# Optimization experiments

Hardware: AMD Instinct MI355X
Metric: run time of the kernel (lower is better)

## Reference

```python
import jax, jax.numpy as jnp
import numpy as np

N = 50000
E = 800000
IN_C, HID, OUT_C, HEADS = 128, 32, 64, 4
NEG_SLOPE = 0.2


def setup_inputs() -> dict:
    key = jax.random.key(0)
    ks = jax.random.split(key, 10)
    x = jax.random.normal(ks[0], (N, IN_C), dtype=jnp.float32)
    edge_index = jax.random.randint(ks[1], (2, E), 0, N, dtype=jnp.int64)
    s = 0.05
    W1 = jax.random.normal(ks[2], (IN_C, HID), dtype=jnp.float32) * s
    b1 = jnp.zeros((HID,), dtype=jnp.float32)
    Wg = jax.random.normal(ks[3], (HID, HEADS * HID), dtype=jnp.float32) * s
    ag_src = jax.random.normal(ks[4], (HEADS, HID), dtype=jnp.float32) * s
    ag_dst = jax.random.normal(ks[5], (HEADS, HID), dtype=jnp.float32) * s
    bg = jnp.zeros((HID,), dtype=jnp.float32)
    W2 = jax.random.normal(ks[6], (HID, OUT_C), dtype=jnp.float32) * s
    b2 = jnp.zeros((OUT_C,), dtype=jnp.float32)
    return {"x": x, "edge_index": edge_index, "W1": W1, "b1": b1,
            "Wg": Wg, "ag_src": ag_src, "ag_dst": ag_dst, "bg": bg,
            "W2": W2, "b2": b2}


def _add_self_loops(edge_index, n):
    loop = jnp.arange(n, dtype=edge_index.dtype)
    return jnp.concatenate([edge_index, jnp.stack([loop, loop])], axis=1)


def _gcn(x, src, dst, W, b, n):
    # PyG GCNConv: symmetric normalization with self-loops, scatter-add
    xw = x @ W  # [N, F]
    deg = jnp.zeros((n,), xw.dtype).at[dst].add(1.0)  # in-degree incl self-loops
    dinv = jax.lax.rsqrt(deg)
    norm = dinv[src] * dinv[dst]  # [E']
    msg = xw[src] * norm[:, None]  # [E', F]
    out = jax.ops.segment_sum(msg, dst, num_segments=n)
    return out + b


def _gat(x, src, dst, Wg, a_src, a_dst, b, n):
    # PyG GATConv, concat=False (mean over heads), leaky_relu slope 0.2
    h = (x @ Wg).reshape(n, HEADS, HID)  # [N, H, D]
    al_s = jnp.einsum('nhd,hd->nh', h, a_src)  # [N, H]
    al_d = jnp.einsum('nhd,hd->nh', h, a_dst)
    logits = jax.nn.leaky_relu(al_s[src] + al_d[dst], NEG_SLOPE)  # [E', H]
    # segment softmax over incoming edges of each dst node
    m = jax.ops.segment_max(logits, dst, num_segments=n)
    e = jnp.exp(logits - m[dst])
    denom = jax.ops.segment_sum(e, dst, num_segments=n)
    alpha = e / denom[dst]  # [E', H]
    msg = h[src] * alpha[:, :, None]  # [E', H, D]
    out = jax.ops.segment_sum(msg, dst, num_segments=n)  # [N, H, D]
    return out.mean(axis=1) + b


def reference(x, edge_index, W1, b1, Wg, ag_src, ag_dst, bg, W2, b2):
    ei = _add_self_loops(edge_index, N)
    src, dst = ei[0], ei[1]
    h = jax.nn.relu(_gcn(x, src, dst, W1, b1, N))
    h = jax.nn.relu(_gat(h, src, dst, Wg, ag_src, ag_dst, bg, N))
    return _gcn(h, src, dst, W2, b2, N)
```

## Files before the change

### kernel.cpp

```cpp
#include <hip/hip_runtime.h>
#include <hip/hip_bf16.h>

#define N_NODES 50000
#define N_EDGES 800000
#define EP (N_EDGES + N_NODES)
#define IN_C 128
#define HID 32
#define OUT_C 64
#define HEADS 4
#define NEG_SLOPE 0.2f

#define NPB 128
#define K_BUCKETS ((N_NODES + NPB - 1) / NPB)

typedef unsigned int uint32;
typedef __attribute__((ext_vector_type(8))) short bf16x8;
typedef __attribute__((ext_vector_type(4))) float f32x4;

__device__ __forceinline__ float bf_lo(uint32 u) { return __uint_as_float(u << 16); }
__device__ __forceinline__ float bf_hi(uint32 u) { return __uint_as_float(u & 0xffff0000u); }
__device__ __forceinline__ uint32 f2bf(float f) {
    uint32 u = __float_as_uint(f);
    return (u + 0x7fffu + ((u >> 16) & 1u)) >> 16;
}
__device__ __forceinline__ uint32 pack_bf2(float a, float b) {
    return f2bf(a) | (f2bf(b) << 16);
}

__global__ __launch_bounds__(512) void k_init2(int* __restrict__ gcnt,
                                               const float* __restrict__ Wg,
                                               const float* __restrict__ ags,
                                               const float* __restrict__ agd,
                                               float* __restrict__ wals,
                                               float* __restrict__ wald,
                                               const float* __restrict__ W2,
                                               uint32* __restrict__ wgB,
                                               uint32* __restrict__ w2B) {
    int t = threadIdx.x;
    if (t < K_BUCKETS + 1) gcnt[t] = 0;
    if (t < 256) {
        int c = t & 127;
        int h = c >> 5, k = c & 31;
        const float* a = (t < 128) ? ags : agd;
        float acc = 0.f;
#pragma unroll
        for (int d = 0; d < 32; d++) acc += Wg[k * 128 + h * 32 + d] * a[h * 32 + d];
        if (t < 128) wals[c] = acc; else wald[c] = acc;
    }
    for (int i = t; i < 2048; i += 512) {
        int tile = i >> 8;
        int T = tile >> 2, kt = tile & 3;
        int r = i & 255;
        int L = r >> 2, di = r & 3;
        int k0 = kt * 32 + (L >> 4) * 8 + 2 * di;
        int k1 = k0 + 1;
        int n = T * 16 + (L & 15);
        float a = Wg[(k0 & 31) * 128 + (k0 >> 5) * 32 + n];
        float b = Wg[(k1 & 31) * 128 + (k1 >> 5) * 32 + n];
        wgB[i] = pack_bf2(a, b);
    }
    for (int i = t; i < 1024; i += 512) {
        int T = i >> 8;
        int r = i & 255;
        int L = r >> 2, di = r & 3;
        int k0 = (L >> 4) * 8 + 2 * di;
        int n = T * 16 + (L & 15);
        w2B[i] = pack_bf2(W2[k0 * 64 + n], W2[(k0 + 1) * 64 + n]);
    }
}


__global__ __launch_bounds__(256) void k_bcount(const int* __restrict__ ei,
                                                int* __restrict__ gcnt) {
    __shared__ int h[K_BUCKETS];
    int t = threadIdx.x;
    for (int i = t; i < K_BUCKETS; i += 256) h[i] = 0;
    __syncthreads();
    int base = blockIdx.x * 4096;
    int dd[16];
#pragma unroll
    for (int k = 0; k < 16; k++) {
        int e = base + k * 256 + t;
        dd[k] = (e < N_EDGES) ? ei[N_EDGES + e] : -1;
    }
#pragma unroll
    for (int k = 0; k < 16; k++)
        if (dd[k] >= 0) atomicAdd(&h[dd[k] >> 7], 1);
    __syncthreads();
    for (int i = t; i < K_BUCKETS; i += 256)
        if (h[i]) atomicAdd(&gcnt[i], h[i]);
}

__global__ __launch_bounds__(512) void k_bscan(const int* __restrict__ gcnt,
                                               int* __restrict__ gbase,
                                               int* __restrict__ gcursor) {
    __shared__ int sd[512];
    int t = threadIdx.x;
    int v = (t < K_BUCKETS) ? gcnt[t] : 0;
    sd[t] = v;
    __syncthreads();
    for (int off = 1; off < 512; off <<= 1) {
        int x = (t >= off) ? sd[t - off] : 0;
        __syncthreads();
        sd[t] += x;
        __syncthreads();
    }
    if (t < K_BUCKETS) {
        int excl = sd[t] - v;
        gbase[t] = excl;
        gcursor[t] = excl;
    }
    if (t == 0) gbase[K_BUCKETS] = sd[K_BUCKETS - 1];
}

__global__ __launch_bounds__(256) void k_bucket(const int* __restrict__ ei,
                                                int* __restrict__ gcursor,
                                                uint32* __restrict__ gpairs) {
    __shared__ int cnt[K_BUCKETS];
    __shared__ int bas[K_BUCKETS];
    int t = threadIdx.x;
    for (int i = t; i < K_BUCKETS; i += 256) cnt[i] = 0;
    __syncthreads();
    int base = blockIdx.x * 2048;
    int ss[8], dd[8], ml[8];
#pragma unroll
    for (int k = 0; k < 8; k++) {
        int e = base + k * 256 + t;
        ss[k] = (e < N_EDGES) ? ei[e] : -1;
        dd[k] = (e < N_EDGES) ? ei[N_EDGES + e] : 0;
    }
#pragma unroll
    for (int k = 0; k < 8; k++)
        if (ss[k] >= 0) ml[k] = atomicAdd(&cnt[dd[k] >> 7], 1);
    __syncthreads();
    for (int i = t; i < K_BUCKETS; i += 256)
        bas[i] = cnt[i] ? atomicAdd(&gcursor[i], cnt[i]) : 0;
    __syncthreads();
#pragma unroll
    for (int k = 0; k < 8; k++)
        if (ss[k] >= 0)
            gpairs[bas[dd[k] >> 7] + ml[k]] = ((uint32)ss[k] << 7) | (uint32)(dd[k] & 127);
}

__global__ __launch_bounds__(256) void k_node(const uint32* __restrict__ gpairs,
                                              const int* __restrict__ gbase,
                                              int* __restrict__ offs,
                                              float* __restrict__ dinv,
                                              int* __restrict__ srcs,
                                              int* __restrict__ perm) {
    __shared__ int cnt[NPB];
    __shared__ int scn[NPB];
    __shared__ int cur[NPB];
    __shared__ unsigned skey[NPB];
    int t = threadIdx.x;
    int b = blockIdx.x;
    int lo = b << 7;
    int nn = N_NODES - lo; if (nn > NPB) nn = NPB;
    int pb = gbase[b], pe = gbase[b + 1];
    if (t < NPB) cnt[t] = 0;
    __syncthreads();
    for (int i = pb + t; i < pe; i += 256)
        atomicAdd(&cnt[gpairs[i] & 127], 1);
    __syncthreads();
    if (t < NPB) scn[t] = cnt[t];
    __syncthreads();
    for (int off = 1; off < NPB; off <<= 1) {
        int x = 0;
        if (t >= off && t < NPB) x = scn[t - off];
        __syncthreads();
        if (t < NPB) scn[t] += x;
        __syncthreads();
    }
    if (t < nn) {
        int excl = scn[t] - cnt[t];
        int o = pb + excl + lo + t;
        offs[lo + t] = o;
        cur[t] = o;
        dinv[lo + t] = rsqrtf((float)(cnt[t] + 1));
        srcs[pb + scn[t] + lo + t] = lo + t;
    }
    if (b == K_BUCKETS - 1 && t == 0) offs[N_NODES] = pe + N_NODES;
    __syncthreads();
    for (int i = pb + t; i < pe; i += 256) {
        uint32 u = gpairs[i];
        int pos = atomicAdd(&cur[u & 127], 1);
        srcs[pos] = (int)(u >> 7);
    }
    if (t < NPB)
        skey[t] = (t < nn) ? (((unsigned)cnt[t] << 7) | (unsigned)t)
                           : (0x7fffff80u | (unsigned)t);
    __syncthreads();
    for (int k = 2; k <= NPB; k <<= 1) {
        for (int jj = k >> 1; jj > 0; jj >>= 1) {
            if (t < NPB) {
                int ixj = t ^ jj;
                if (ixj > t) {
                    unsigned a = skey[t], bb = skey[ixj];
                    if (((t & k) == 0) ? (a > bb) : (a < bb)) {
                        skey[t] = bb; skey[ixj] = a;
                    }
                }
            }
            __syncthreads();
        }
    }
    if (t < nn) perm[lo + t] = lo + (int)(skey[t] & 127u);
}

__global__ __launch_bounds__(256) void k_gemm1(const float* __restrict__ x,
                                               const float* __restrict__ W1,
                                               const float* __restrict__ dinv,
                                               uint32* __restrict__ xw1) {
    __shared__ float wl[IN_C * HID];
    __shared__ float xl[8 * IN_C];
    int t = threadIdx.x;
    for (int i = t; i < IN_C * HID; i += 256) {
        int k = i >> 5, f = i & 31;
        wl[(k >> 1) * 64 + f * 2 + (k & 1)] = W1[i];
    }
    int nb = blockIdx.x * 8;
    const float4* x4 = (const float4*)(x + (size_t)nb * IN_C);
    ((float4*)xl)[t] = x4[t];
    __syncthreads();
    int g = t >> 5, f = t & 31;
    const float2* xr = (const float2*)(xl + g * IN_C);
    const float2* wp = (const float2*)wl;
    float acc = 0.f;
#pragma unroll 16
    for (int k2 = 0; k2 < 64; k2++) {
        float2 xv = xr[k2];
        float2 wv = wp[k2 * 32 + f];
        acc += xv.x * wv.x + xv.y * wv.y;
    }
    float v = acc * dinv[nb + g];
    float vn = __shfl_xor(v, 1, 64);
    if ((f & 1) == 0) xw1[(size_t)(nb + g) * 16 + (f >> 1)] = pack_bf2(v, vn);
}

__global__ __launch_bounds__(256) void k_gather1(const uint32* __restrict__ xw1,
                                                 const int* __restrict__ offs,
                                                 const int* __restrict__ srcs,
                                                 const int* __restrict__ perm,
                                                 const float* __restrict__ dinv,
                                                 const float* __restrict__ b1,
                                                 const float* __restrict__ wals,
                                                 const float* __restrict__ wald,
                                                 char* __restrict__ rec) {
    int t = threadIdx.x;
    int l16 = t & 15;
    int n = perm[blockIdx.x * 16 + (t >> 4)];
    int s0 = offs[n], s1 = offs[n + 1];
    const char* xb = (const char*)xw1 + l16 * 4;
    float a0 = 0.f, a1 = 0.f, a2 = 0.f, a3 = 0.f;
    float a4 = 0.f, a5 = 0.f, a6 = 0.f, a7 = 0.f;
    int j = s0;
    for (; j + 3 < s1; j += 4) {
        uint32 uA = *(const uint32*)(xb + ((uint32)srcs[j] << 6));
        uint32 uB = *(const uint32*)(xb + ((uint32)srcs[j + 1] << 6));
        uint32 uC = *(const uint32*)(xb + ((uint32)srcs[j + 2] << 6));
        uint32 uD = *(const uint32*)(xb + ((uint32)srcs[j + 3] << 6));
        a0 += bf_lo(uA); a1 += bf_hi(uA);
        a2 += bf_lo(uB); a3 += bf_hi(uB);
        a4 += bf_lo(uC); a5 += bf_hi(uC);
        a6 += bf_lo(uD); a7 += bf_hi(uD);
    }
    for (; j < s1; ++j) {
        uint32 uA = *(const uint32*)(xb + ((uint32)srcs[j] << 6));
        a0 += bf_lo(uA); a1 += bf_hi(uA);
    }
    float dn = dinv[n];
    float2 b = ((const float2*)b1)[l16];
    float vx = ((a0 + a2) + (a4 + a6)) * dn + b.x;
    float vy = ((a1 + a3) + (a5 + a7)) * dn + b.y;
    vx = vx > 0.f ? vx : 0.f;
    vy = vy > 0.f ? vy : 0.f;
    char* rn = rec + (size_t)n * 128;
    *(uint32*)(rn + l16 * 4) = pack_bf2(vx, vy);

    float ps0, ps1, ps2, ps3, pd0, pd1, pd2, pd3;
    {
        float2 w0 = ((const float2*)wals)[0 * 16 + l16];
        float2 w1 = ((const float2*)wals)[1 * 16 + l16];
        float2 w2 = ((const float2*)wals)[2 * 16 + l16];
        float2 w3 = ((const float2*)wals)[3 * 16 + l16];
        ps0 = vx * w0.x + vy * w0.y;
        ps1 = vx * w1.x + vy * w1.y;
        ps2 = vx * w2.x + vy * w2.y;
        ps3 = vx * w3.x + vy * w3.y;
        float2 u0 = ((const float2*)wald)[0 * 16 + l16];
        float2 u1 = ((const float2*)wald)[1 * 16 + l16];
        float2 u2 = ((const float2*)wald)[2 * 16 + l16];
        float2 u3 = ((const float2*)wald)[3 * 16 + l16];
        pd0 = vx * u0.x + vy * u0.y;
        pd1 = vx * u1.x + vy * u1.y;
        pd2 = vx * u2.x + vy * u2.y;
        pd3 = vx * u3.x + vy * u3.y;
    }
#pragma unroll
    for (int m = 1; m < 16; m <<= 1) {
        ps0 += __shfl_xor(ps0, m, 16); ps1 += __shfl_xor(ps1, m, 16);
        ps2 += __shfl_xor(ps2, m, 16); ps3 += __shfl_xor(ps3, m, 16);
        pd0 += __shfl_xor(pd0, m, 16); pd1 += __shfl_xor(pd1, m, 16);
        pd2 += __shfl_xor(pd2, m, 16); pd3 += __shfl_xor(pd3, m, 16);
    }
    if (l16 == 0) {
        float4* r4 = (float4*)rn;
        r4[4] = make_float4(ps0, ps1, ps2, ps3);
        r4[5] = make_float4(pd0, pd1, pd2, pd3);
    }
}

__global__ __launch_bounds__(512) void k_gat_agg(const char* __restrict__ rec,
                                                 const int* __restrict__ offs,
                                                 const int* __restrict__ srcs,
                                                 const int* __restrict__ perm,
                                                 const uint32* __restrict__ wgB,
                                                 const float* __restrict__ bg,
                                                 const float* __restrict__ dinv,
                                                 uint32* __restrict__ h2s) {
    __shared__ __align__(16) uint32 gl[16][64];
    int t = threadIdx.x;
    int l32 = t & 31;
    int g8 = t >> 5;
    int n = perm[blockIdx.x * 16 + g8];
    int l16 = l32 & 15;
    int par = l32 >> 4;
    int s0 = offs[n], s1 = offs[n + 1];
    float4 dv = ((const float4*)(rec + (size_t)n * 128))[5];
    uint32 hoff = l16 * 4;

    float g00 = 0.f, g01 = 0.f, g10 = 0.f, g11 = 0.f;
    float g20 = 0.f, g21 = 0.f, g30 = 0.f, g31 = 0.f;
    float ss0 = 0.f, ss1 = 0.f, ss2 = 0.f, ss3 = 0.f;

#define GAT_EDGE(J)                                                            \
    {                                                                          \
        uint32 off = (uint32)srcs[J] << 7;                                     \
        float4 ev = *(const float4*)(rec + off + 64);                          \
        uint32 u = *(const uint32*)(rec + off + hoff);                         \
        float flo = bf_lo(u), fhi = bf_hi(u);                                  \
        float tt, w;                                                           \
        tt = ev.x + dv.x; w = __expf(fmaxf(tt, NEG_SLOPE * tt));               \
        ss0 += w; g00 += w * flo; g01 += w * fhi;                              \
        tt = ev.y + dv.y; w = __expf(fmaxf(tt, NEG_SLOPE * tt));               \
        ss1 += w; g10 += w * flo; g11 += w * fhi;                              \
        tt = ev.z + dv.z; w = __expf(fmaxf(tt, NEG_SLOPE * tt));               \
        ss2 += w; g20 += w * flo; g21 += w * fhi;                              \
        tt = ev.w + dv.w; w = __expf(fmaxf(tt, NEG_SLOPE * tt));               \
        ss3 += w; g30 += w * flo; g31 += w * fhi;                              \
    }

    int j = s0 + par;
    for (; j + 2 < s1; j += 4) {
        GAT_EDGE(j);
        GAT_EDGE(j + 2);
    }
    if (j < s1) GAT_EDGE(j);
#undef GAT_EDGE

    ss0 += __shfl_xor(ss0, 16, 64); ss1 += __shfl_xor(ss1, 16, 64);
    ss2 += __shfl_xor(ss2, 16, 64); ss3 += __shfl_xor(ss3, 16, 64);
    g00 += __shfl_xor(g00, 16, 64); g01 += __shfl_xor(g01, 16, 64);
    g10 += __shfl_xor(g10, 16, 64); g11 += __shfl_xor(g11, 16, 64);
    g20 += __shfl_xor(g20, 16, 64); g21 += __shfl_xor(g21, 16, 64);
    g30 += __shfl_xor(g30, 16, 64); g31 += __shfl_xor(g31, 16, 64);
    float i0 = 0.25f / ss0, i1 = 0.25f / ss1, i2 = 0.25f / ss2, i3 = 0.25f / ss3;
    if (l32 < 16) {
        gl[g8][0 * 16 + l16] = pack_bf2(g00 * i0, g01 * i0);
        gl[g8][1 * 16 + l16] = pack_bf2(g10 * i1, g11 * i1);
        gl[g8][2 * 16 + l16] = pack_bf2(g20 * i2, g21 * i2);
        gl[g8][3 * 16 + l16] = pack_bf2(g30 * i3, g31 * i3);
    }
    __syncthreads();
    if (t < 64) {
        int L = t;
        int mA = L & 15;
        int quad = L >> 4;
        int nbase = blockIdx.x * 16;
        int pn[4];
        float dns[4];
#pragma unroll
        for (int r = 0; r < 4; r++) {
            pn[r] = perm[nbase + quad * 4 + r];
            dns[r] = dinv[pn[r]];
        }
#pragma unroll
        for (int T = 0; T < 2; T++) {
            f32x4 acc = {0.f, 0.f, 0.f, 0.f};
#pragma unroll
            for (int kt = 0; kt < 4; kt++) {
                bf16x8 af = *(const bf16x8*)&gl[mA][kt * 16 + quad * 4];
                bf16x8 bf = *(const bf16x8*)(wgB + (size_t)((T * 4 + kt) * 64 + L) * 4);
                acc = __builtin_amdgcn_mfma_f32_16x16x32_bf16(af, bf, acc, 0, 0, 0);
            }
            int d = T * 16 + (L & 15);
            float bgd = bg[d];
#pragma unroll
            for (int r = 0; r < 4; r++) {
                float v = acc[r] + bgd;
                v = v > 0.f ? v : 0.f;
                v *= dns[r];
                float vn = __shfl_xor(v, 1, 64);
                if ((d & 1) == 0)
                    h2s[(size_t)pn[r] * 16 + (d >> 1)] = pack_bf2(v, vn);
            }
        }
    }
}

__global__ __launch_bounds__(256) void k_gather2(const uint32* __restrict__ h2s,
                                                 const int* __restrict__ offs,
                                                 const int* __restrict__ srcs,
                                                 const int* __restrict__ perm,
                                                 const uint32* __restrict__ w2B,
                                                 const float* __restrict__ dinv,
                                                 const float* __restrict__ b2,
                                                 float* __restrict__ out) {
    __shared__ __align__(16) uint32 gbf[16][16];
    int t = threadIdx.x;
    int l16 = t & 15;
    int g16 = t >> 4;
    int n = perm[blockIdx.x * 16 + g16];
    int s0 = offs[n], s1 = offs[n + 1];
    const char* xb = (const char*)h2s + l16 * 4;
    float a0 = 0.f, a1 = 0.f, a2 = 0.f, a3 = 0.f;
    float a4 = 0.f, a5 = 0.f, a6 = 0.f, a7 = 0.f;
    int j = s0;
    for (; j + 3 < s1; j += 4) {
        uint32 uA = *(const uint32*)(xb + ((uint32)srcs[j] << 6));
        uint32 uB = *(const uint32*)(xb + ((uint32)srcs[j + 1] << 6));
        uint32 uC = *(const uint32*)(xb + ((uint32)srcs[j + 2] << 6));
        uint32 uD = *(const uint32*)(xb + ((uint32)srcs[j + 3] << 6));
        a0 += bf_lo(uA); a1 += bf_hi(uA);
        a2 += bf_lo(uB); a3 += bf_hi(uB);
        a4 += bf_lo(uC); a5 += bf_hi(uC);
        a6 += bf_lo(uD); a7 += bf_hi(uD);
    }
    for (; j < s1; ++j) {
        uint32 uA = *(const uint32*)(xb + ((uint32)srcs[j] << 6));
        a0 += bf_lo(uA); a1 += bf_hi(uA);
    }
    gbf[g16][l16] = pack_bf2((a0 + a2) + (a4 + a6), (a1 + a3) + (a5 + a7));
    __syncthreads();
    if (t < 64) {
        int L = t;
        int quad = L >> 4;
        int nbase = blockIdx.x * 16;
        int pn[4];
        float dns[4];
#pragma unroll
        for (int r = 0; r < 4; r++) {
            pn[r] = perm[nbase + quad * 4 + r];
            dns[r] = dinv[pn[r]];
        }
        bf16x8 af = *(const bf16x8*)&gbf[L & 15][quad * 4];
#pragma unroll
        for (int T = 0; T < 4; T++) {
            bf16x8 bf = *(const bf16x8*)(w2B + (size_t)(T * 64 + L) * 4);
            f32x4 acc = {0.f, 0.f, 0.f, 0.f};
            acc = __builtin_amdgcn_mfma_f32_16x16x32_bf16(af, bf, acc, 0, 0, 0);
            int d = T * 16 + (L & 15);
            float b2d = b2[d];
#pragma unroll
            for (int r = 0; r < 4; r++) {
                out[(size_t)pn[r] * OUT_C + d] = acc[r] * dns[r] + b2d;
            }
        }
    }
}

extern "C" void kernel_launch(void* const* d_in, const int* in_sizes, int n_in,
                              void* d_out, int out_size, void* d_ws, size_t ws_size,
                              hipStream_t stream) {
    const float* x   = (const float*)d_in[0];
    const int*   ei  = (const int*)d_in[1];
    const float* W1  = (const float*)d_in[2];
    const float* b1  = (const float*)d_in[3];
    const float* Wg  = (const float*)d_in[4];
    const float* ags = (const float*)d_in[5];
    const float* agd = (const float*)d_in[6];
    const float* bg  = (const float*)d_in[7];
    const float* W2  = (const float*)d_in[8];
    const float* b2  = (const float*)d_in[9];
    float* out = (float*)d_out;

    char* p = (char*)d_ws;
    auto alloc = [&](size_t bytes) -> void* {
        void* r = (void*)p;
        p += (bytes + 255) & ~(size_t)255;
        return r;
    };
    float*  dinv    = (float*)alloc((size_t)N_NODES * 4);
    int*    offs    = (int*)  alloc((size_t)(N_NODES + 1) * 4);
    int*    gcnt    = (int*)  alloc((size_t)(K_BUCKETS + 1) * 4);
    int*    gbase   = (int*)  alloc((size_t)(K_BUCKETS + 1) * 4);
    int*    gcursor = (int*)  alloc((size_t)(K_BUCKETS + 1) * 4);
    int*    srcs    = (int*)  alloc((size_t)EP * 4);
    uint32* gpairs  = (uint32*)alloc((size_t)N_EDGES * 4);
    uint32* xw1     = (uint32*)alloc((size_t)N_NODES * 16 * 4);
    char*   rec     = (char*) alloc((size_t)N_NODES * 128);
    float*  wals    = (float*)alloc(128 * 4);
    float*  wald    = (float*)alloc(128 * 4);
    uint32* wgB     = (uint32*)alloc(2048 * 4);
    uint32* w2B     = (uint32*)alloc(1024 * 4);
    uint32* h2s     = (uint32*)alloc((size_t)N_NODES * 16 * 4);
    int*    perm    = (int*)  alloc((size_t)N_NODES * 4);

    k_init2<<<1, 512, 0, stream>>>(gcnt, Wg, ags, agd, wals, wald, W2, wgB, w2B);
    k_bcount<<<(N_EDGES + 4095) / 4096, 256, 0, stream>>>(ei, gcnt);
    k_bscan<<<1, 512, 0, stream>>>(gcnt, gbase, gcursor);
    k_bucket<<<(N_EDGES + 2047) / 2048, 256, 0, stream>>>(ei, gcursor, gpairs);
    k_node<<<K_BUCKETS, 256, 0, stream>>>(gpairs, gbase, offs, dinv, srcs, perm);

    k_gemm1<<<N_NODES / 8, 256, 0, stream>>>(x, W1, dinv, xw1);
    k_gather1<<<N_NODES / 16, 256, 0, stream>>>(xw1, offs, srcs, perm, dinv, b1,
                                                wals, wald, rec);

    k_gat_agg<<<N_NODES / 16, 512, 0, stream>>>(rec, offs, srcs, perm, wgB, bg,
                                                dinv, h2s);

    k_gather2<<<N_NODES / 16, 256, 0, stream>>>(h2s, offs, srcs, perm, w2B,
                                                dinv, b2, out);
}
```

Baseline: 219.8 us.

## Vectorize neighbor gathers by splitting lanes across edges and feature chunks

The three gather kernels (GCN layer 1, GAT aggregation, GCN layer 2) now split each node's lane group between several edges in parallel and a feature slice per lane. Each lane issues 16-byte (GCN) or 8-byte (GAT) loads instead of 4-byte loads, and cross-edge partial sums are combined with shuffles. The aim is fewer, wider memory transactions per gathered row and more edges in flight at once, which matters for these latency-bound random gathers. In exchange it adds shuffle reductions, a predicated tail that reads srcs past the edge range (the buffer is padded to allow this), and more accumulator registers in the GAT kernel.

```diff
diff --git a/kernel.cpp b/kernel.cpp
--- a/kernel.cpp
+++ b/kernel.cpp
@@ -248,65 +248,67 @@
                                                  char* __restrict__ rec) {
     int t = threadIdx.x;
     int l16 = t & 15;
+    int es = l16 >> 2;
+    int q  = l16 & 3;
     int n = perm[blockIdx.x * 16 + (t >> 4)];
     int s0 = offs[n], s1 = offs[n + 1];
-    const char* xb = (const char*)xw1 + l16 * 4;
     float a0 = 0.f, a1 = 0.f, a2 = 0.f, a3 = 0.f;
     float a4 = 0.f, a5 = 0.f, a6 = 0.f, a7 = 0.f;
-    int j = s0;
-    for (; j + 3 < s1; j += 4) {
-        uint32 uA = *(const uint32*)(xb + ((uint32)srcs[j] << 6));
-        uint32 uB = *(const uint32*)(xb + ((uint32)srcs[j + 1] << 6));
-        uint32 uC = *(const uint32*)(xb + ((uint32)srcs[j + 2] << 6));
-        uint32 uD = *(const uint32*)(xb + ((uint32)srcs[j + 3] << 6));
-        a0 += bf_lo(uA); a1 += bf_hi(uA);
-        a2 += bf_lo(uB); a3 += bf_hi(uB);
-        a4 += bf_lo(uC); a5 += bf_hi(uC);
-        a6 += bf_lo(uD); a7 += bf_hi(uD);
-    }
-    for (; j < s1; ++j) {
-        uint32 uA = *(const uint32*)(xb + ((uint32)srcs[j] << 6));
-        a0 += bf_lo(uA); a1 += bf_hi(uA);
-    }
+#pragma unroll 2
+    for (int j = s0; j < s1; j += 4) {
+        int je = j + es;
+        int sidx = srcs[je];
+        if (je < s1) {
+            uint4 u = *(const uint4*)((const char*)xw1 + ((uint32)sidx << 6) + q * 16);
+            a0 += bf_lo(u.x); a1 += bf_hi(u.x);
+            a2 += bf_lo(u.y); a3 += bf_hi(u.y);
+            a4 += bf_lo(u.z); a5 += bf_hi(u.z);
+            a6 += bf_lo(u.w); a7 += bf_hi(u.w);
+        }
+    }
+#define RED_ES(v) v += __shfl_xor(v, 4, 64); v += __shfl_xor(v, 8, 64);
+    RED_ES(a0) RED_ES(a1) RED_ES(a2) RED_ES(a3)
+    RED_ES(a4) RED_ES(a5) RED_ES(a6) RED_ES(a7)
+#undef RED_ES
     float dn = dinv[n];
-    float2 b = ((const float2*)b1)[l16];
-    float vx = ((a0 + a2) + (a4 + a6)) * dn + b.x;
-    float vy = ((a1 + a3) + (a5 + a7)) * dn + b.y;
-    vx = vx > 0.f ? vx : 0.f;
-    vy = vy > 0.f ? vy : 0.f;
+    float4 bA = ((const float4*)b1)[2 * q];
+    float4 bB = ((const float4*)b1)[2 * q + 1];
+    float v0 = a0 * dn + bA.x, v1 = a1 * dn + bA.y;
+    float v2 = a2 * dn + bA.z, v3 = a3 * dn + bA.w;
+    float v4 = a4 * dn + bB.x, v5 = a5 * dn + bB.y;
+    float v6 = a6 * dn + bB.z, v7 = a7 * dn + bB.w;
+    v0 = v0 > 0.f ? v0 : 0.f; v1 = v1 > 0.f ? v1 : 0.f;
+    v2 = v2 > 0.f ? v2 : 0.f; v3 = v3 > 0.f ? v3 : 0.f;
+    v4 = v4 > 0.f ? v4 : 0.f; v5 = v5 > 0.f ? v5 : 0.f;
+    v6 = v6 > 0.f ? v6 : 0.f; v7 = v7 > 0.f ? v7 : 0.f;
     char* rn = rec + (size_t)n * 128;
-    *(uint32*)(rn + l16 * 4) = pack_bf2(vx, vy);
-
-    float ps0, ps1, ps2, ps3, pd0, pd1, pd2, pd3;
-    {
-        float2 w0 = ((const float2*)wals)[0 * 16 + l16];
-        float2 w1 = ((const float2*)wals)[1 * 16 + l16];
-        float2 w2 = ((const float2*)wals)[2 * 16 + l16];
-        float2 w3 = ((const float2*)wals)[3 * 16 + l16];
-        ps0 = vx * w0.x + vy * w0.y;
-        ps1 = vx * w1.x + vy * w1.y;
-        ps2 = vx * w2.x + vy * w2.y;
-        ps3 = vx * w3.x + vy * w3.y;
-        float2 u0 = ((const float2*)wald)[0 * 16 + l16];
-        float2 u1 = ((const float2*)wald)[1 * 16 + l16];
-        float2 u2 = ((const float2*)wald)[2 * 16 + l16];
-        float2 u3 = ((const float2*)wald)[3 * 16 + l16];
-        pd0 = vx * u0.x + vy * u0.y;
-        pd1 = vx * u1.x + vy * u1.y;
-        pd2 = vx * u2.x + vy * u2.y;
-        pd3 = vx * u3.x + vy * u3.y;
-    }
-#pragma unroll
-    for (int m = 1; m < 16; m <<= 1) {
-        ps0 += __shfl_xor(ps0, m, 16); ps1 += __shfl_xor(ps1, m, 16);
-        ps2 += __shfl_xor(ps2, m, 16); ps3 += __shfl_xor(ps3, m, 16);
-        pd0 += __shfl_xor(pd0, m, 16); pd1 += __shfl_xor(pd1, m, 16);
-        pd2 += __shfl_xor(pd2, m, 16); pd3 += __shfl_xor(pd3, m, 16);
+    if (es == 0) {
+        uint4 w;
+        w.x = pack_bf2(v0, v1); w.y = pack_bf2(v2, v3);
+        w.z = pack_bf2(v4, v5); w.w = pack_bf2(v6, v7);
+        *(uint4*)(rn + q * 16) = w;
+    }
+    float ps[4], pd[4];
+#pragma unroll
+    for (int h = 0; h < 4; h++) {
+        const float4* wa = (const float4*)(wals + h * 32 + 8 * q);
+        float4 wv0 = wa[0], wv1 = wa[1];
+        ps[h] = v0 * wv0.x + v1 * wv0.y + v2 * wv0.z + v3 * wv0.w
+              + v4 * wv1.x + v5 * wv1.y + v6 * wv1.z + v7 * wv1.w;
+        const float4* wb = (const float4*)(wald + h * 32 + 8 * q);
+        float4 uv0 = wb[0], uv1 = wb[1];
+        pd[h] = v0 * uv0.x + v1 * uv0.y + v2 * uv0.z + v3 * uv0.w
+              + v4 * uv1.x + v5 * uv1.y + v6 * uv1.z + v7 * uv1.w;
+    }
+#pragma unroll
+    for (int h = 0; h < 4; h++) {
+        ps[h] += __shfl_xor(ps[h], 1, 64); ps[h] += __shfl_xor(ps[h], 2, 64);
+        pd[h] += __shfl_xor(pd[h], 1, 64); pd[h] += __shfl_xor(pd[h], 2, 64);
     }
     if (l16 == 0) {
         float4* r4 = (float4*)rn;
-        r4[4] = make_float4(ps0, ps1, ps2, ps3);
-        r4[5] = make_float4(pd0, pd1, pd2, pd3);
+        r4[4] = make_float4(ps[0], ps[1], ps[2], ps[3]);
+        r4[5] = make_float4(pd[0], pd[1], pd[2], pd[3]);
     }
 }
 
@@ -323,53 +325,56 @@
     int l32 = t & 31;
     int g8 = t >> 5;
     int n = perm[blockIdx.x * 16 + g8];
-    int l16 = l32 & 15;
-    int par = l32 >> 4;
+    int es = l32 >> 3;
+    int q  = l32 & 7;
     int s0 = offs[n], s1 = offs[n + 1];
     float4 dv = ((const float4*)(rec + (size_t)n * 128))[5];
-    uint32 hoff = l16 * 4;
-
-    float g00 = 0.f, g01 = 0.f, g10 = 0.f, g11 = 0.f;
-    float g20 = 0.f, g21 = 0.f, g30 = 0.f, g31 = 0.f;
+
+    float g00 = 0.f, g01 = 0.f, g02 = 0.f, g03 = 0.f;
+    float g10 = 0.f, g11 = 0.f, g12 = 0.f, g13 = 0.f;
+    float g20 = 0.f, g21 = 0.f, g22 = 0.f, g23 = 0.f;
+    float g30 = 0.f, g31 = 0.f, g32 = 0.f, g33 = 0.f;
     float ss0 = 0.f, ss1 = 0.f, ss2 = 0.f, ss3 = 0.f;
 
-#define GAT_EDGE(J)                                                            \
-    {                                                                          \
-        uint32 off = (uint32)srcs[J] << 7;                                     \
-        float4 ev = *(const float4*)(rec + off + 64);                          \
-        uint32 u = *(const uint32*)(rec + off + hoff);                         \
-        float flo = bf_lo(u), fhi = bf_hi(u);                                  \
-        float tt, w;                                                           \
-        tt = ev.x + dv.x; w = __expf(fmaxf(tt, NEG_SLOPE * tt));               \
-        ss0 += w; g00 += w * flo; g01 += w * fhi;                              \
-        tt = ev.y + dv.y; w = __expf(fmaxf(tt, NEG_SLOPE * tt));               \
-        ss1 += w; g10 += w * flo; g11 += w * fhi;                              \
-        tt = ev.z + dv.z; w = __expf(fmaxf(tt, NEG_SLOPE * tt));               \
-        ss2 += w; g20 += w * flo; g21 += w * fhi;                              \
-        tt = ev.w + dv.w; w = __expf(fmaxf(tt, NEG_SLOPE * tt));               \
-        ss3 += w; g30 += w * flo; g31 += w * fhi;                              \
-    }
-
-    int j = s0 + par;
-    for (; j + 2 < s1; j += 4) {
-        GAT_EDGE(j);
-        GAT_EDGE(j + 2);
-    }
-    if (j < s1) GAT_EDGE(j);
-#undef GAT_EDGE
-
-    ss0 += __shfl_xor(ss0, 16, 64); ss1 += __shfl_xor(ss1, 16, 64);
-    ss2 += __shfl_xor(ss2, 16, 64); ss3 += __shfl_xor(ss3, 16, 64);
-    g00 += __shfl_xor(g00, 16, 64); g01 += __shfl_xor(g01, 16, 64);
-    g10 += __shfl_xor(g10, 16, 64); g11 += __shfl_xor(g11, 16, 64);
-    g20 += __shfl_xor(g20, 16, 64); g21 += __shfl_xor(g21, 16, 64);
-    g30 += __shfl_xor(g30, 16, 64); g31 += __shfl_xor(g31, 16, 64);
+#pragma unroll 2
+    for (int j = s0; j < s1; j += 4) {
+        int je = j + es;
+        int sidx = srcs[je];
+        if (je < s1) {
+            uint32 off = (uint32)sidx << 7;
+            float4 ev = *(const float4*)(rec + off + 64);
+            uint2 u = *(const uint2*)(rec + off + q * 8);
+            float f0 = bf_lo(u.x), f1 = bf_hi(u.x);
+            float f2 = bf_lo(u.y), f3 = bf_hi(u.y);
+            float tt, w;
+            tt = ev.x + dv.x; w = __expf(fmaxf(tt, NEG_SLOPE * tt));
+            ss0 += w; g00 += w * f0; g01 += w * f1; g02 += w * f2; g03 += w * f3;
+            tt = ev.y + dv.y; w = __expf(fmaxf(tt, NEG_SLOPE * tt));
+            ss1 += w; g10 += w * f0; g11 += w * f1; g12 += w * f2; g13 += w * f3;
+            tt = ev.z + dv.z; w = __expf(fmaxf(tt, NEG_SLOPE * tt));
+            ss2 += w; g20 += w * f0; g21 += w * f1; g22 += w * f2; g23 += w * f3;
+            tt = ev.w + dv.w; w = __expf(fmaxf(tt, NEG_SLOPE * tt));
+            ss3 += w; g30 += w * f0; g31 += w * f1; g32 += w * f2; g33 += w * f3;
+        }
+    }
+#define RED_ES(v) v += __shfl_xor(v, 8, 64); v += __shfl_xor(v, 16, 64);
+    RED_ES(ss0) RED_ES(ss1) RED_ES(ss2) RED_ES(ss3)
+    RED_ES(g00) RED_ES(g01) RED_ES(g02) RED_ES(g03)
+    RED_ES(g10) RED_ES(g11) RED_ES(g12) RED_ES(g13)
+    RED_ES(g20) RED_ES(g21) RED_ES(g22) RED_ES(g23)
+    RED_ES(g30) RED_ES(g31) RED_ES(g32) RED_ES(g33)
+#undef RED_ES
     float i0 = 0.25f / ss0, i1 = 0.25f / ss1, i2 = 0.25f / ss2, i3 = 0.25f / ss3;
-    if (l32 < 16) {
-        gl[g8][0 * 16 + l16] = pack_bf2(g00 * i0, g01 * i0);
-        gl[g8][1 * 16 + l16] = pack_bf2(g10 * i1, g11 * i1);
-        gl[g8][2 * 16 + l16] = pack_bf2(g20 * i2, g21 * i2);
-        gl[g8][3 * 16 + l16] = pack_bf2(g30 * i3, g31 * i3);
+    if (es == 0) {
+        uint2 w;
+        w.x = pack_bf2(g00 * i0, g01 * i0); w.y = pack_bf2(g02 * i0, g03 * i0);
+        *(uint2*)&gl[g8][0 * 16 + 2 * q] = w;
+        w.x = pack_bf2(g10 * i1, g11 * i1); w.y = pack_bf2(g12 * i1, g13 * i1);
+        *(uint2*)&gl[g8][1 * 16 + 2 * q] = w;
+        w.x = pack_bf2(g20 * i2, g21 * i2); w.y = pack_bf2(g22 * i2, g23 * i2);
+        *(uint2*)&gl[g8][2 * 16 + 2 * q] = w;
+        w.x = pack_bf2(g30 * i3, g31 * i3); w.y = pack_bf2(g32 * i3, g33 * i3);
+        *(uint2*)&gl[g8][3 * 16 + 2 * q] = w;
     }
     __syncthreads();
     if (t < 64) {
@@ -419,28 +424,35 @@
     __shared__ __align__(16) uint32 gbf[16][16];
     int t = threadIdx.x;
     int l16 = t & 15;
+    int es = l16 >> 2;
+    int q  = l16 & 3;
     int g16 = t >> 4;
     int n = perm[blockIdx.x * 16 + g16];
     int s0 = offs[n], s1 = offs[n + 1];
-    const char* xb = (const char*)h2s + l16 * 4;
     float a0 = 0.f, a1 = 0.f, a2 = 0.f, a3 = 0.f;
     float a4 = 0.f, a5 = 0.f, a6 = 0.f, a7 = 0.f;
-    int j = s0;
-    for (; j + 3 < s1; j += 4) {
-        uint32 uA = *(const uint32*)(xb + ((uint32)srcs[j] << 6));
-        uint32 uB = *(const uint32*)(xb + ((uint32)srcs[j + 1] << 6));
-        uint32 uC = *(const uint32*)(xb + ((uint32)srcs[j + 2] << 6));
-        uint32 uD = *(const uint32*)(xb + ((uint32)srcs[j + 3] << 6));
-        a0 += bf_lo(uA); a1 += bf_hi(uA);
-        a2 += bf_lo(uB); a3 += bf_hi(uB);
-        a4 += bf_lo(uC); a5 += bf_hi(uC);
-        a6 += bf_lo(uD); a7 += bf_hi(uD);
-    }
-    for (; j < s1; ++j) {
-        uint32 uA = *(const uint32*)(xb + ((uint32)srcs[j] << 6));
-        a0 += bf_lo(uA); a1 += bf_hi(uA);
-    }
-    gbf[g16][l16] = pack_bf2((a0 + a2) + (a4 + a6), (a1 + a3) + (a5 + a7));
+#pragma unroll 2
+    for (int j = s0; j < s1; j += 4) {
+        int je = j + es;
+        int sidx = srcs[je];
+        if (je < s1) {
+            uint4 u = *(const uint4*)((const char*)h2s + ((uint32)sidx << 6) + q * 16);
+            a0 += bf_lo(u.x); a1 += bf_hi(u.x);
+            a2 += bf_lo(u.y); a3 += bf_hi(u.y);
+            a4 += bf_lo(u.z); a5 += bf_hi(u.z);
+            a6 += bf_lo(u.w); a7 += bf_hi(u.w);
+        }
+    }
+#define RED_ES(v) v += __shfl_xor(v, 4, 64); v += __shfl_xor(v, 8, 64);
+    RED_ES(a0) RED_ES(a1) RED_ES(a2) RED_ES(a3)
+    RED_ES(a4) RED_ES(a5) RED_ES(a6) RED_ES(a7)
+#undef RED_ES
+    if (es == 0) {
+        uint4 w;
+        w.x = pack_bf2(a0, a1); w.y = pack_bf2(a2, a3);
+        w.z = pack_bf2(a4, a5); w.w = pack_bf2(a6, a7);
+        *(uint4*)&gbf[g16][4 * q] = w;
+    }
     __syncthreads();
     if (t < 64) {
         int L = t;
@@ -495,7 +507,7 @@
     int*    gcnt    = (int*)  alloc((size_t)(K_BUCKETS + 1) * 4);
     int*    gbase   = (int*)  alloc((size_t)(K_BUCKETS + 1) * 4);
     int*    gcursor = (int*)  alloc((size_t)(K_BUCKETS + 1) * 4);
-    int*    srcs    = (int*)  alloc((size_t)EP * 4);
+    int*    srcs    = (int*)  alloc((size_t)(EP + 8) * 4);
     uint32* gpairs  = (uint32*)alloc((size_t)N_EDGES * 4);
     uint32* xw1     = (uint32*)alloc((size_t)N_NODES * 16 * 4);
     char*   rec     = (char*) alloc((size_t)N_NODES * 128);
```

Result: no change. 221.8 us (+0.9%).
